# Kernel tuning notes

Measured on AMD Instinct MI355X. Metric: run time of the kernel, lower is better.

The kernel has to match this reference:

```python
import jax, jax.numpy as jnp
import numpy as np

NBITS = 4
GROUP = 128
K = 4096   # in_features
N = 4096   # out_features
M = 4096   # flattened batch*seq tokens
EPS = 32 // NBITS  # elements per packed int32 = 8
MASK = (1 << NBITS) - 1  # unpack_mask = 15


def setup_inputs() -> dict:
    key = jax.random.key(0)
    k1, k2, k3, k4, k5 = jax.random.split(key, 5)
    x = jax.random.normal(k1, (M, K), dtype=jnp.float32)
    # raw 4-bit quantized weights, layout [K, N] (i.e. W_q.t() from the torch module)
    nib = jax.random.randint(k2, (K, N), 0, 1 << NBITS, dtype=jnp.int32)
    # pack EPS nibbles per int32 along K, matching pack(): element j gets shift j*NBITS
    nib = nib.reshape(K // EPS, EPS, N)
    shifts = (jnp.arange(EPS, dtype=jnp.int32) * NBITS)[None, :, None]
    parts = nib << shifts  # disjoint bit ranges
    W_q_packed = parts[:, 0]
    for j in range(1, EPS):
        W_q_packed = W_q_packed | parts[:, j]
    W_q_packed = W_q_packed.astype(jnp.int32)  # [K//EPS, N]
    # group-wise scales/zeros: [K//GROUP, N] (scales.view(N,-1).t() layout)
    scales = (jax.random.uniform(k3, (K // GROUP, N), dtype=jnp.float32) + 0.5) * 0.01
    zeros = jax.random.uniform(k4, (K // GROUP, N), dtype=jnp.float32) * MASK
    bias = jax.random.normal(k5, (N,), dtype=jnp.float32) * 0.1
    return {"x": x, "W_q_packed": W_q_packed, "scales": scales, "zeros": zeros, "bias": bias}


def reference(x, W_q_packed, scales, zeros, bias):
    # unpack: w[k, n] = (packed[k//EPS, n] >> ((k % EPS) * NBITS)) & MASK
    shifts = (jnp.arange(EPS, dtype=jnp.int32) * NBITS)[None, :, None]
    w = (W_q_packed[:, None, :] >> shifts) & MASK  # [K//EPS, EPS, N]
    w = w.reshape(K, N).astype(jnp.float32)
    # group-wise asymmetric dequant (W_group_mode == 3): W = (w - z) * s
    s = jnp.repeat(scales, GROUP, axis=0)  # [K, N]
    z = jnp.repeat(zeros, GROUP, axis=0)   # [K, N]
    W = (w - z) * s
    out = x @ W + bias  # [M, N]
    return out
```

## Files before the change

### kernel.cpp

```cpp
#include <hip/hip_runtime.h>
#include <stdint.h>


#define M_DIM 4096
#define N_DIM 4096
#define K_DIM 4096

typedef __attribute__((ext_vector_type(8))) short short8;
typedef __attribute__((ext_vector_type(4))) float f32x4;

__device__ __forceinline__ unsigned short f2bf(float f) {
  uint32_t u = __builtin_bit_cast(uint32_t, f);
  u += 0x7fffu + ((u >> 16) & 1u);
  return (unsigned short)(u >> 16);
}

__global__ __launch_bounds__(256) void cvt_x_kernel(const float* __restrict__ x,
                                                    unsigned short* __restrict__ xb) {
  const int total = (M_DIM * K_DIM) / 4;
  const float4* x4 = (const float4*)x;
  ushort4* o4 = (ushort4*)xb;
  for (int i = blockIdx.x * 256 + threadIdx.x; i < total; i += gridDim.x * 256) {
    float4 v = x4[i];
    ushort4 o;
    o.x = f2bf(v.x); o.y = f2bf(v.y); o.z = f2bf(v.z); o.w = f2bf(v.w);
    o4[i] = o;
  }
}

__global__ __launch_bounds__(256) void dequant_kernel(const int* __restrict__ Wq,
                                                      const float* __restrict__ scales,
                                                      const float* __restrict__ zeros,
                                                      unsigned short* __restrict__ wt) {
  __shared__ uint4 Ts[32 * 64];
  const int tid = threadIdx.x;
  const int n0 = blockIdx.x * 32;
  const int gk0 = blockIdx.y * 64;

#pragma unroll
  for (int p = 0; p < 8; ++p) {
    int e = p * 256 + tid;
    int n_l = e & 31;
    int gk_l = e >> 5;
    int gk = gk0 + gk_l;
    int n = n0 + n_l;
    int g = gk >> 4;
    uint32_t q = (uint32_t)Wq[gk * N_DIM + n];
    float s = scales[g * N_DIM + n];
    float z = zeros[g * N_DIM + n];
    unsigned short b[8];
#pragma unroll
    for (int j = 0; j < 8; ++j) {
      float f = ((float)((q >> (4 * j)) & 15u) - z) * s;
      b[j] = f2bf(f);
    }
    uint4 cell;
    cell.x = (uint32_t)b[0] | ((uint32_t)b[1] << 16);
    cell.y = (uint32_t)b[2] | ((uint32_t)b[3] << 16);
    cell.z = (uint32_t)b[4] | ((uint32_t)b[5] << 16);
    cell.w = (uint32_t)b[6] | ((uint32_t)b[7] << 16);
    Ts[n_l * 64 + (gk_l ^ (n_l & 7))] = cell;
  }
  __syncthreads();
  uint4* dst = (uint4*)wt;
#pragma unroll
  for (int p = 0; p < 8; ++p) {
    int n_l = p * 4 + (tid >> 6);
    int gk_l = tid & 63;
    uint4 cell = Ts[n_l * 64 + (gk_l ^ (n_l & 7))];
    dst[(size_t)(n0 + n_l) * (K_DIM / 8) + (gk0 + gk_l)] = cell;
  }
}

__global__ __launch_bounds__(256) void gemm_bt_kernel(const unsigned short* __restrict__ A,
                                                      const unsigned short* __restrict__ Bt,
                                                      const float* __restrict__ bias,
                                                      float* __restrict__ C) {
  __shared__ short8 As[1024];
  __shared__ short8 Bs[1024];
  const int tid = threadIdx.x;
  const int lane = tid & 63;
  const int w = tid >> 6;
  const int wm = w >> 1, wn = w & 1;
  const int m0 = blockIdx.y * 128;
  const int n0 = blockIdx.x * 128;

  const int c0 = w * 256 + lane;
  const int row0 = c0 >> 3;
  const int kcx0 = c0 & 7;
  const int kc0 = kcx0 ^ (row0 & 7);
  const unsigned short* Ablk = A + (size_t)m0 * K_DIM;
  const unsigned short* Bblk = Bt + (size_t)n0 * K_DIM;
  const int voff = row0 * K_DIM + kc0 * 8;

  f32x4 acc[4][4] = {};

  const int fr = lane & 15;
  const int fc = lane >> 4;
  const int a_row8 = (wm * 64 + fr) * 8;
  const int b_row8 = (wn * 64 + fr) * 8;
  const int kx0 = fc ^ (fr & 7);
  const int kx1 = (4 + fc) ^ (fr & 7);

  for (int kk = 0; kk < K_DIM / 64; ++kk) {
    const int k0 = kk * 64;
    __syncthreads();
#pragma unroll
    for (int j = 0; j < 4; ++j) {
      __builtin_amdgcn_global_load_lds(
          (const __attribute__((address_space(1))) void*)(Ablk + voff + j * 8 * K_DIM + k0),
          (__attribute__((address_space(3))) void*)&As[c0 + j * 64], 16, 0, 0);
      __builtin_amdgcn_global_load_lds(
          (const __attribute__((address_space(1))) void*)(Bblk + voff + j * 8 * K_DIM + k0),
          (__attribute__((address_space(3))) void*)&Bs[c0 + j * 64], 16, 0, 0);
    }
    __syncthreads();

    {
      short8 af[4], bv[4];
#pragma unroll
      for (int mi = 0; mi < 4; ++mi) af[mi] = As[a_row8 + mi * 128 + kx0];
#pragma unroll
      for (int ni = 0; ni < 4; ++ni) bv[ni] = Bs[b_row8 + ni * 128 + kx0];
#pragma unroll
      for (int mi = 0; mi < 4; ++mi)
#pragma unroll
        for (int ni = 0; ni < 4; ++ni)
          acc[mi][ni] = __builtin_amdgcn_mfma_f32_16x16x32_bf16(af[mi], bv[ni], acc[mi][ni], 0, 0, 0);
    }
    {
      short8 af[4], bv[4];
#pragma unroll
      for (int mi = 0; mi < 4; ++mi) af[mi] = As[a_row8 + mi * 128 + kx1];
#pragma unroll
      for (int ni = 0; ni < 4; ++ni) bv[ni] = Bs[b_row8 + ni * 128 + kx1];
#pragma unroll
      for (int mi = 0; mi < 4; ++mi)
#pragma unroll
        for (int ni = 0; ni < 4; ++ni)
          acc[mi][ni] = __builtin_amdgcn_mfma_f32_16x16x32_bf16(af[mi], bv[ni], acc[mi][ni], 0, 0, 0);
    }
  }

  const int rr = (lane >> 4) * 4;
#pragma unroll
  for (int ni = 0; ni < 4; ++ni) {
    const int gn = n0 + wn * 64 + ni * 16 + fr;
    const float bvv = bias[gn];
#pragma unroll
    for (int mi = 0; mi < 4; ++mi) {
      const int gm = m0 + wm * 64 + mi * 16 + rr;
#pragma unroll
      for (int r = 0; r < 4; ++r)
        C[(size_t)(gm + r) * N_DIM + gn] = acc[mi][ni][r] + bvv;
    }
  }
}

extern "C" void kernel_launch(void* const* d_in, const int* in_sizes, int n_in,
                              void* d_out, int out_size, void* d_ws, size_t ws_size,
                              hipStream_t stream) {
  const float* x = (const float*)d_in[0];
  const int* wq = (const int*)d_in[1];
  const float* sc = (const float*)d_in[2];
  const float* zr = (const float*)d_in[3];
  const float* bias = (const float*)d_in[4];
  float* out = (float*)d_out;

  unsigned short* xb = (unsigned short*)d_ws;
  unsigned short* wt = (unsigned short*)((char*)d_ws + (size_t)M_DIM * K_DIM * 2);

  cvt_x_kernel<<<dim3(2048), dim3(256), 0, stream>>>(x, xb);
  dequant_kernel<<<dim3(N_DIM / 32, (K_DIM / 8) / 64), dim3(256), 0, stream>>>(wq, sc, zr, wt);
  gemm_bt_kernel<<<dim3(N_DIM / 128, M_DIM / 128), dim3(256), 0, stream>>>(xb, wt, bias, out);
}
```

Before: 288.4 us.

## Merge x-conversion and dequant kernels; remap GEMM tiles for XCD locality

Combines the fp32-to-bf16 activation conversion and the weight dequantization into one launch, split by block index, so one kernel launch and its tail are removed and the two memory-bound jobs can overlap. The conversion now handles eight elements per thread. The GEMM grid becomes 1D, and each block index is remapped so blocks placed on the same XCD share N tiles, which is meant to improve L2 reuse of the weight tiles. The remapping assumes round-robin dispatch of blocks across the eight XCDs.

Measured after the change: 285.3 us. Within noise of the previous version (-1.1%).

```diff
diff --git a/kernel.cpp b/kernel.cpp
--- a/kernel.cpp
+++ b/kernel.cpp
@@ -15,27 +15,36 @@
   return (unsigned short)(u >> 16);
 }
 
-__global__ __launch_bounds__(256) void cvt_x_kernel(const float* __restrict__ x,
-                                                    unsigned short* __restrict__ xb) {
-  const int total = (M_DIM * K_DIM) / 4;
-  const float4* x4 = (const float4*)x;
-  ushort4* o4 = (ushort4*)xb;
-  for (int i = blockIdx.x * 256 + threadIdx.x; i < total; i += gridDim.x * 256) {
-    float4 v = x4[i];
-    ushort4 o;
-    o.x = f2bf(v.x); o.y = f2bf(v.y); o.z = f2bf(v.z); o.w = f2bf(v.w);
-    o4[i] = o;
-  }
-}
-
-__global__ __launch_bounds__(256) void dequant_kernel(const int* __restrict__ Wq,
-                                                      const float* __restrict__ scales,
-                                                      const float* __restrict__ zeros,
-                                                      unsigned short* __restrict__ wt) {
+__global__ __launch_bounds__(256) void prep_kernel(const float* __restrict__ x,
+                                                   unsigned short* __restrict__ xb,
+                                                   const int* __restrict__ Wq,
+                                                   const float* __restrict__ scales,
+                                                   const float* __restrict__ zeros,
+                                                   unsigned short* __restrict__ wt) {
   __shared__ uint4 Ts[32 * 64];
   const int tid = threadIdx.x;
-  const int n0 = blockIdx.x * 32;
-  const int gk0 = blockIdx.y * 64;
+  if (blockIdx.x < 2048) {
+    const int total = (M_DIM * K_DIM) / 8;
+    const float4* x4 = (const float4*)x;
+    uint4* o8 = (uint4*)xb;
+#pragma unroll
+    for (int p = 0; p < 4; ++p) {
+      int i = (p * 2048 + blockIdx.x) * 256 + tid;
+      if (i < total) {
+        float4 a = x4[2 * i], b = x4[2 * i + 1];
+        uint4 o;
+        o.x = (uint32_t)f2bf(a.x) | ((uint32_t)f2bf(a.y) << 16);
+        o.y = (uint32_t)f2bf(a.z) | ((uint32_t)f2bf(a.w) << 16);
+        o.z = (uint32_t)f2bf(b.x) | ((uint32_t)f2bf(b.y) << 16);
+        o.w = (uint32_t)f2bf(b.z) | ((uint32_t)f2bf(b.w) << 16);
+        o8[i] = o;
+      }
+    }
+    return;
+  }
+  const int blk = blockIdx.x - 2048;
+  const int n0 = (blk & 127) * 32;
+  const int gk0 = (blk >> 7) * 64;
 
 #pragma unroll
   for (int p = 0; p < 8; ++p) {
@@ -82,13 +91,18 @@
   const int lane = tid & 63;
   const int w = tid >> 6;
   const int wm = w >> 1, wn = w & 1;
-  const int m0 = blockIdx.y * 128;
-  const int n0 = blockIdx.x * 128;
+
+  const int b = blockIdx.x;
+  const int xcd = b & 7;
+  const int loc = b >> 3;
+  const int nt = xcd * 4 + (loc & 3);
+  const int mt = loc >> 2;
+  const int m0 = mt * 128;
+  const int n0 = nt * 128;
 
   const int c0 = w * 256 + lane;
   const int row0 = c0 >> 3;
-  const int kcx0 = c0 & 7;
-  const int kc0 = kcx0 ^ (row0 & 7);
+  const int kc0 = (c0 & 7) ^ (row0 & 7);
   const unsigned short* Ablk = A + (size_t)m0 * K_DIM;
   const unsigned short* Bblk = Bt + (size_t)n0 * K_DIM;
   const int voff = row0 * K_DIM + kc0 * 8;
@@ -170,7 +184,6 @@
   unsigned short* xb = (unsigned short*)d_ws;
   unsigned short* wt = (unsigned short*)((char*)d_ws + (size_t)M_DIM * K_DIM * 2);
 
-  cvt_x_kernel<<<dim3(2048), dim3(256), 0, stream>>>(x, xb);
-  dequant_kernel<<<dim3(N_DIM / 32, (K_DIM / 8) / 64), dim3(256), 0, stream>>>(wq, sc, zr, wt);
-  gemm_bt_kernel<<<dim3(N_DIM / 128, M_DIM / 128), dim3(256), 0, stream>>>(xb, wt, bias, out);
+  prep_kernel<<<dim3(3072), dim3(256), 0, stream>>>(x, xb, wq, sc, zr, wt);
+  gemm_bt_kernel<<<dim3(1024), dim3(256), 0, stream>>>(xb, wt, bias, out);
 }
```
